# Kernel optimization log

Hardware: AMD Instinct MI355X
Metric: run time of the kernel (lower is better)

The kernel has to match this reference:

```python
import jax, jax.numpy as jnp
import numpy as np

NCA_HIDDEN = 16
N_CODES = 32
EMBED_DIM = 64


def conv2d(x, w, pad, b=None):
    # x: (N, Cin, H, W), w: (Cout, Cin, kh, kw)
    y = jax.lax.conv_general_dilated(
        x, w, window_strides=(1, 1), padding=[(pad, pad), (pad, pad)],
        dimension_numbers=('NCHW', 'OIHW', 'NCHW'))
    if b is not None:
        y = y + b[None, :, None, None]
    return y


def setup_inputs() -> dict:
    key = jax.random.key(0)
    ks = jax.random.split(key, 32)
    rn = lambda k, shp, s=0.05: jax.random.normal(k, shp, dtype=jnp.float32) * s
    H = NCA_HIDDEN
    upd = H * H * 3 * 3  # 2304
    tau = H * H          # 256
    inp = {
        'demo_inputs':  jax.random.normal(ks[0], (8, 1, 64, 64), dtype=jnp.float32),
        'demo_outputs': jax.random.normal(ks[1], (8, 1, 64, 64), dtype=jnp.float32),
        'test_input':   jax.random.normal(ks[2], (16, 1, 256, 256), dtype=jnp.float32),
        # TaskEncoder params
        'enc_w1': rn(ks[3], (16, 2, 3, 3)),  'enc_b1': jnp.zeros((16,), jnp.float32),
        'enc_w2': rn(ks[4], (32, 16, 3, 3)), 'enc_b2': jnp.zeros((32,), jnp.float32),
        'enc_lw': rn(ks[5], (EMBED_DIM, 32)), 'enc_lb': jnp.zeros((EMBED_DIM,), jnp.float32),
        # gen_update hypernet
        'gu_w1': rn(ks[6], (128, EMBED_DIM)), 'gu_b1': jnp.zeros((128,), jnp.float32),
        'gu_w2': rn(ks[7], (upd, 128)),       'gu_b2': jnp.zeros((upd,), jnp.float32),
        # gen_tau hypernet
        'gt_w1': rn(ks[8], (64, EMBED_DIM)),  'gt_b1': jnp.zeros((64,), jnp.float32),
        'gt_w2': rn(ks[9], (tau, 64)),        'gt_b2': jnp.zeros((tau,), jnp.float32),
        # stem
        'stem_w': rn(ks[10], (H, 1, 3, 3)), 'stem_b': jnp.zeros((H,), jnp.float32),
        # VQ codebook, init U(-1/n_codes, 1/n_codes)
        'codebook': jax.random.uniform(ks[11], (N_CODES, H), jnp.float32,
                                       minval=-1.0 / N_CODES, maxval=1.0 / N_CODES),
        # decoder 1x1 conv
        'dec_w': rn(ks[12], (1, H, 1, 1)), 'dec_b': jnp.zeros((1,), jnp.float32),
        'n_steps': 5,
    }
    return inp


def reference(demo_inputs, demo_outputs, test_input,
              enc_w1, enc_b1, enc_w2, enc_b2, enc_lw, enc_lb,
              gu_w1, gu_b1, gu_w2, gu_b2,
              gt_w1, gt_b1, gt_w2, gt_b2,
              stem_w, stem_b, codebook, dec_w, dec_b, n_steps):
    H = NCA_HIDDEN
    # --- Task encoder: mean task embedding over demo pairs ---
    pairs = jnp.concatenate([demo_inputs, demo_outputs], axis=1)  # (N,2,h,w)
    h = jax.nn.relu(conv2d(pairs, enc_w1, 1, enc_b1))
    h = jax.nn.relu(conv2d(h, enc_w2, 1, enc_b2))
    h = h.mean(axis=(2, 3))                   # AdaptiveAvgPool2d(1)+Flatten -> (N,32)
    te = (h @ enc_lw.T + enc_lb).mean(axis=0)  # (embed_dim,)
    # --- Hypernetworks generate NCA weights ---
    W_update = (jax.nn.relu(te @ gu_w1.T + gu_b1) @ gu_w2.T + gu_b2).reshape(H, H, 3, 3)
    W_tau = (jax.nn.relu(te @ gt_w1.T + gt_b1) @ gt_w2.T + gt_b2).reshape(H, H, 1, 1)
    # --- Stem ---
    state = jax.nn.relu(conv2d(test_input, stem_w, 1, stem_b))  # (B,16,Hh,Ww)
    cb_sq = (codebook ** 2).sum(axis=1)  # (n_codes,)
    for _ in range(int(n_steps)):
        delta = jax.nn.relu(conv2d(state, W_update, 1))
        beta = jax.nn.sigmoid(conv2d(state, W_tau, 0))
        state = beta * state + (1.0 - beta) * delta
        # --- VQ step (straight-through) ---
        B, C, Hh, Ww = state.shape
        zf = state.transpose(0, 2, 3, 1).reshape(-1, C)  # (B*Hh*Ww, C)
        dists = (zf ** 2).sum(1, keepdims=True) + cb_sq - 2.0 * (zf @ codebook.T)
        idx = jnp.argmin(dists, axis=1)
        zq = codebook[idx].reshape(B, Hh, Ww, C).transpose(0, 3, 1, 2)
        state = state + jax.lax.stop_gradient(zq - state)
    output = jax.nn.sigmoid(conv2d(state, dec_w, 0, dec_b))
    return output
```

## Files before the change

kernel.cpp:

```cpp
#include <hip/hip_runtime.h>
#include <stdint.h>

#define NPIX 65536
#define NIMG 16

typedef float4 F4;
typedef _Float16 h2v __attribute__((ext_vector_type(2)));
typedef _Float16 h8v __attribute__((ext_vector_type(8)));
typedef float    f4v __attribute__((ext_vector_type(4)));

union H8 { h8v v; h2v p[4]; _Float16 e[8]; };

__device__ __forceinline__ float sigm(float x){ return 1.0f/(1.0f+__expf(-x)); }

#if defined(__has_builtin)
#if __has_builtin(__builtin_amdgcn_rcpf)
#define FRCP(x) __builtin_amdgcn_rcpf(x)
#endif
#endif
#ifndef FRCP
#define FRCP(x) (1.0f/(x))
#endif
__device__ __forceinline__ float sigmf(float x){ return FRCP(1.0f + __expf(-x)); }

__device__ __forceinline__ h2v pkrtz(float a, float b){
  return __builtin_bit_cast(h2v, __builtin_amdgcn_cvt_pkrtz(a,b));
}

#if defined(__has_builtin)
#if __has_builtin(__builtin_amdgcn_fdot2)
#define FDOT2(a,b,c) __builtin_amdgcn_fdot2((a),(b),(c),false)
#endif
#endif
#ifndef FDOT2
#define FDOT2(a,b,c) ((c) + (float)(a)[0]*(float)(b)[0] + (float)(a)[1]*(float)(b)[1])
#endif

__global__ __launch_bounds__(256) void k_prep(
    const float* __restrict__ w2, _Float16* __restrict__ wfragE,
    float* __restrict__ pooled)
{
  int t=threadIdx.x;
  pooled[t]=0.f;
  for(int i=t;i<5120;i+=256){
    int j=i&7, rest=i>>3, lane=rest&63, rest2=rest>>6, ks=rest2%5, b=rest2/5;
    int g=lane>>4, nn=lane&15;
    int k=32*ks+8*g+j;
    float v=0.f;
    if(k<144){
      int tap=2*ks+(g>>1), ci=8*(g&1)+j, co=b*16+nn;
      v=w2[co*144+ci*9+tap];
    }
    wfragE[i]=(_Float16)v;
  }
}

__global__ __launch_bounds__(256) void k_enc(
    const float* __restrict__ din, const float* __restrict__ dou,
    const float* __restrict__ w1, const float* __restrict__ b1,
    const float* __restrict__ b2,
    const _Float16* __restrict__ wfragE,
    float* __restrict__ pooled)
{
  __shared__ float2 in_s[400];
  __shared__ h8v st_h[324*3];
  __shared__ float red[4][32];
  __shared__ h2v stwp_s[144];
  __shared__ h2v stbp_s[8];

  const int tid=threadIdx.x;
  const int bx=blockIdx.x, by=blockIdx.y, n=blockIdx.z;
  const float* i0 = din + n*4096;
  const float* i1 = dou + n*4096;

  for(int i=tid;i<400;i+=256){
    int sy=i/20, sx=i-sy*20;
    int gy=by*16-2+sy, gx=bx*16-2+sx;
    bool ok=((unsigned)gy<64u && (unsigned)gx<64u);
    in_s[i] = ok ? make_float2(i0[gy*64+gx], i1[gy*64+gx]) : make_float2(0.f,0.f);
  }
  if(tid<144){
    int q=tid/18, r=tid-18*q;
    stwp_s[tid]=pkrtz(w1[36*q+r], w1[36*q+18+r]);
  } else if(tid<152){
    int q=tid-144;
    stbp_s[q]=pkrtz(b1[2*q], b1[2*q+1]);
  }

  const int lane=tid&63, w=tid>>6, g=lane>>4, nn=lane&15;
  h8v B0[5], B1[5];
  const h8v* wfE=(const h8v*)wfragE;
  #pragma unroll
  for(int ks=0;ks<5;ks++){ B0[ks]=wfE[ks*64+lane]; B1[ks]=wfE[(5+ks)*64+lane]; }
  float b2a=b2[nn], b2b=b2[nn+16];
  __syncthreads();

  for(int p=tid;p<324;p+=256){
    int syh=p/18, sxh=p-syh*18;
    int gy=by*16-1+syh, gx=bx*16-1+sxh;
    H8 o0,o1;
    if((unsigned)gy<64u && (unsigned)gx<64u){
      h2v a2[8];
      #pragma unroll
      for(int q=0;q<8;q++) a2[q]=stbp_s[q];
      #pragma unroll
      for(int ky=0;ky<3;ky++){
        #pragma unroll
        for(int kx=0;kx<3;kx++){
          int tp=ky*3+kx;
          float2 v=in_s[(syh+ky)*20+(sxh+kx)];
          h2v v0=pkrtz(v.x,v.x), v1=pkrtz(v.y,v.y);
          #pragma unroll
          for(int q=0;q<8;q++){
            a2[q]=stwp_s[(2*q)*9+tp]*v0 + a2[q];
            a2[q]=stwp_s[(2*q+1)*9+tp]*v1 + a2[q];
          }
        }
      }
      o0.p[0]=a2[0]; o0.p[1]=a2[1]; o0.p[2]=a2[2]; o0.p[3]=a2[3];
      o1.p[0]=a2[4]; o1.p[1]=a2[5]; o1.p[2]=a2[6]; o1.p[3]=a2[7];
      #pragma unroll
      for(int c=0;c<8;c++){
        o0.e[c]=o0.e[c]>(_Float16)0?o0.e[c]:(_Float16)0;
        o1.e[c]=o1.e[c]>(_Float16)0?o1.e[c]:(_Float16)0;
      }
    } else {
      o0.v=(h8v){0,0,0,0,0,0,0,0};
      o1.v=(h8v){0,0,0,0,0,0,0,0};
    }
    st_h[p*3]  =o0.v;
    st_h[p*3+1]=o1.v;
  }
  __syncthreads();

  f4v acc0[4], acc1[4];
  #pragma unroll
  for(int m=0;m<4;m++){ acc0[m]=(f4v){0.f,0.f,0.f,0.f}; acc1[m]=(f4v){0.f,0.f,0.f,0.f}; }
  #pragma unroll
  for(int ks=0;ks<5;ks++){
    int t=2*ks+(g>>1); if(t>8) t=8;
    int tyo=(t*11)>>5, txo=t-tyo*3;
    int sel=g&1;
    #pragma unroll
    for(int m=0;m<4;m++){
      int sy=4*w+m+tyo;
      h8v a=st_h[(sy*18+nn+txo)*3+sel];
      acc0[m]=__builtin_amdgcn_mfma_f32_16x16x32_f16(a,B0[ks],acc0[m],0,0,0);
      acc1[m]=__builtin_amdgcn_mfma_f32_16x16x32_f16(a,B1[ks],acc1[m],0,0,0);
    }
  }
  float s0=0.f, s1=0.f;
  #pragma unroll
  for(int m=0;m<4;m++)
    #pragma unroll
    for(int r=0;r<4;r++){
      s0+=fmaxf(acc0[m][r]+b2a,0.f);
      s1+=fmaxf(acc1[m][r]+b2b,0.f);
    }
  s0+=__shfl_down(s0,32,64); s0+=__shfl_down(s0,16,64);
  s1+=__shfl_down(s1,32,64); s1+=__shfl_down(s1,16,64);
  if(lane<16){ red[w][nn]=s0; red[w][nn+16]=s1; }
  __syncthreads();
  if(tid<32){
    float s=red[0][tid]+red[1][tid]+red[2][tid]+red[3][tid];
    atomicAdd(&pooled[n*32+tid], s);
  }
}

__global__ __launch_bounds__(256) void k_hyper(
    const float* __restrict__ pooled,
    const float* __restrict__ lw, const float* __restrict__ lb,
    const float* __restrict__ guw1, const float* __restrict__ gub1,
    const float* __restrict__ gtw1, const float* __restrict__ gtb1,
    const float* __restrict__ gtw2, const float* __restrict__ gtb2,
    const float* __restrict__ guw2, const float* __restrict__ gub2,
    const float* __restrict__ cb, const float* __restrict__ decw, const float* __restrict__ decb,
    _Float16* __restrict__ wfrag_g,
    _Float16* __restrict__ Mh_g,
    _Float16* __restrict__ bcb_g, _Float16* __restrict__ omb_g,
    _Float16* __restrict__ cbh_g,
    float* __restrict__ chs_g, float* __restrict__ dvals_g)
{
  __shared__ float hm[32], te_s[64], hx_s[128];
  __shared__ float wz_s[256];
  __shared__ float cb_s[512];
  const int t=threadIdx.x, blk=blockIdx.x;
  if(t<32){
    float s=0.f;
    for(int n=0;n<8;n++) s += pooled[n*32+t];
    hm[t] = s * (1.0f/32768.0f);
  }
  for(int i=t;i<512;i+=256) cb_s[i]=cb[i];
  if(blk==9){
    for(int i=t;i<5120;i+=256){
      int j=i&7, rest=i>>3, lane=rest&63, rest2=rest>>6, ks=rest2%5, b=rest2/5;
      int k=32*ks+8*(lane>>4)+j;
      bool pad = (b==0) ? (k>=144) : ((k>>4)!=4);
      if(pad) wfrag_g[i]=(_Float16)0.f;
    }
    for(int i=t;i<264;i+=256){ int k=i>>3, q=i&7; Mh_g[k*152+144+q]=(_Float16)0.f; }
    for(int i=t;i<144;i+=256) Mh_g[32*152+i]=(_Float16)0.f;
  }
  __syncthreads();
  if(t<64){
    float s=lb[t];
    for(int c=0;c<32;c++) s = fmaf(lw[t*32+c], hm[c], s);
    te_s[t]=s;
  }
  __syncthreads();
  if(blk<9){
    if(t<128){
      float s=gub1[t];
      for(int j=0;j<64;j++) s = fmaf(guw1[t*64+j], te_s[j], s);
      hx_s[t]=fmaxf(s,0.f);
    }
    __syncthreads();
    const int ci=t>>4, co=t&15, tp=blk;
    const int o=co*144+ci*9+tp;
    float s=gub2[o];
    const F4* gp=(const F4*)(guw2+(size_t)o*128);
    #pragma unroll
    for(int i=0;i<32;i++){
      F4 g=gp[i];
      s=fmaf(g.x,hx_s[4*i],s); s=fmaf(g.y,hx_s[4*i+1],s);
      s=fmaf(g.z,hx_s[4*i+2],s); s=fmaf(g.w,hx_s[4*i+3],s);
    }
    wz_s[ci*16+co]=s;
    {
      int k=tp*16+ci;
      int ks=k>>5, rem=k&31, g2=rem>>3, j=rem&7, lane=(g2<<4)|co;
      wfrag_g[(ks*64+lane)*8+j]=(_Float16)s;
    }
    __syncthreads();
    for(int o2=t;o2<512;o2+=256){
      int k=o2>>4, c=o2&15;
      float m=0.f;
      for(int c2=0;c2<16;c2++) m=fmaf(wz_s[c2*16+c], cb_s[k*16+c2], m);
      Mh_g[k*152+tp*16+c]=(_Float16)m;
    }
  } else {
    if(t<64){
      float s=gtb1[t];
      for(int j=0;j<64;j++) s = fmaf(gtw1[t*64+j], te_s[j], s);
      hx_s[t]=fmaxf(s,0.f);
    }
    __syncthreads();
    {
      float s=gtb2[t];
      for(int i=0;i<64;i++) s = fmaf(gtw2[t*64+i], hx_s[i], s);
      int co=t>>4, ci=t&15;
      wz_s[ci*16+co]=s;
    }
    __syncthreads();
    {
      int ci=t>>4, co=t&15;
      int g=ci>>3, j=ci&7, lane=(g<<4)|co;
      wfrag_g[(448+lane)*8+j]=(_Float16)wz_s[ci*16+co];
    }
    for(int o=t;o<512;o+=256){
      int k=o>>4, c=o&15;
      float T=0.f;
      for(int ci=0;ci<16;ci++) T = fmaf(wz_s[ci*16+c], cb_s[k*16+ci], T);
      float beta=sigm(T);
      bcb_g[o]=(_Float16)(beta*cb_s[o]);
      omb_g[o]=(_Float16)(1.f-beta);
      cbh_g[o]=(_Float16)cb_s[o];
    }
    if(t<32){
      float sq=0.f, d=0.f;
      for(int c=0;c<16;c++){ float v=cb_s[t*16+c]; sq=fmaf(v,v,sq); d=fmaf(decw[c],v,d); }
      chs_g[t]=0.5f*sq;
      dvals_g[t]=sigm(d+decb[0]);
    }
  }
}

#define ST_STRIDE 3
struct S1P1 { h8v st[324*ST_STRIDE]; float in[400]; };
union S1U { S1P1 p; unsigned int dt[256*20]; };

__global__ __launch_bounds__(256) void k_step1(
    const float* __restrict__ tin,
    const float* __restrict__ stw, const float* __restrict__ stb,
    const _Float16* __restrict__ wfrag,
    const _Float16* __restrict__ cbh, const float* __restrict__ chs,
    uint8_t* __restrict__ idx_out)
{
  __shared__ S1U u;
  __shared__ h8v cb8_s[64];
  __shared__ float chs_s[32];
  __shared__ h2v stwp_s[72];
  __shared__ h2v stbp_s[8];

  const int tid=threadIdx.x;
  const int bx=blockIdx.x, by=blockIdx.y, n=blockIdx.z;
  const float* in = tin + (size_t)n*NPIX;

  for(int i=tid;i<400;i+=256){
    int sy=i/20, sx=i-sy*20;
    int gy=by*16-2+sy, gx=bx*16-2+sx;
    u.p.in[i] = ((unsigned)gy<256u && (unsigned)gx<256u) ? in[gy*256+gx] : 0.0f;
  }
  if(tid<72){
    int q=tid/9, tp=tid-q*9;
    stwp_s[q*9+tp]=pkrtz(stw[(2*q)*9+tp], stw[(2*q+1)*9+tp]);
  } else if(tid<80){
    int q=tid-72;
    stbp_s[q]=pkrtz(stb[2*q], stb[2*q+1]);
  } else if(tid>=160 && tid<192) chs_s[tid-160]=chs[tid-160];
  if(tid<64) ((uint4*)cb8_s)[tid] = ((const uint4*)cbh)[tid];

  const int lane = tid & 63, w = tid >> 6;
  const int g = lane >> 4, nn = lane & 15;
  h8v Bd[5], Bt2;
  const h8v* wf = (const h8v*)wfrag;
  #pragma unroll
  for(int ks=0;ks<5;ks++) Bd[ks]=wf[ks*64+lane];
  Bt2 = wf[7*64+lane];

  __syncthreads();

  for(int p=tid;p<324;p+=256){
    int syh=p/18, sxh=p-syh*18;
    int gy=by*16-1+syh, gx=bx*16-1+sxh;
    H8 b0,b1;
    if((unsigned)gy<256u && (unsigned)gx<256u){
      h2v a2[8];
      #pragma unroll
      for(int q=0;q<8;q++) a2[q]=stbp_s[q];
      #pragma unroll
      for(int ky=0;ky<3;ky++){
        #pragma unroll
        for(int kx=0;kx<3;kx++){
          int tp=ky*3+kx;
          float v=u.p.in[(syh+ky)*20+(sxh+kx)];
          h2v vv=pkrtz(v,v);
          #pragma unroll
          for(int q=0;q<8;q++) a2[q] = stwp_s[q*9+tp]*vv + a2[q];
        }
      }
      b0.p[0]=a2[0]; b0.p[1]=a2[1]; b0.p[2]=a2[2]; b0.p[3]=a2[3];
      b1.p[0]=a2[4]; b1.p[1]=a2[5]; b1.p[2]=a2[6]; b1.p[3]=a2[7];
      #pragma unroll
      for(int c=0;c<8;c++){
        b0.e[c]=b0.e[c]>(_Float16)0?b0.e[c]:(_Float16)0;
        b1.e[c]=b1.e[c]>(_Float16)0?b1.e[c]:(_Float16)0;
      }
    } else {
      b0.v=(h8v){0,0,0,0,0,0,0,0};
      b1.v=(h8v){0,0,0,0,0,0,0,0};
    }
    u.p.st[p*ST_STRIDE]  =b0.v;
    u.p.st[p*ST_STRIDE+1]=b1.v;
  }
  __syncthreads();

  f4v accd[4], acct[4];
  #pragma unroll
  for(int m=0;m<4;m++){ accd[m]=(f4v){0.f,0.f,0.f,0.f}; acct[m]=(f4v){0.f,0.f,0.f,0.f}; }
  #pragma unroll
  for(int ks=0;ks<5;ks++){
    int t = 2*ks + (g>>1); if(t>8) t=8;
    int tyo=(t*11)>>5, txo=t-tyo*3;
    int sel = g&1;
    #pragma unroll
    for(int m=0;m<4;m++){
      int sy = 4*w+m+tyo;
      h8v a = u.p.st[(sy*18 + nn + txo)*ST_STRIDE + sel];
      accd[m]=__builtin_amdgcn_mfma_f32_16x16x32_f16(a,Bd[ks],accd[m],0,0,0);
      if(ks==2) acct[m]=__builtin_amdgcn_mfma_f32_16x16x32_f16(a,Bt2,acct[m],0,0,0);
    }
  }
  const int py=tid>>4, pxx=tid&15;
  const int cpx=((py+1)*18+pxx+1)*ST_STRIDE;
  h8v z0=u.p.st[cpx], z1=u.p.st[cpx+1];
  __syncthreads();

  #pragma unroll
  for(int m=0;m<4;m++){
    #pragma unroll
    for(int r=0;r<4;r++){
      int px=(4*w+m)*16 + g*4 + r;
      h2v pk = pkrtz(accd[m][r], acct[m][r]);
      u.dt[px*20+nn] = __builtin_bit_cast(unsigned int, pk);
    }
  }
  __syncthreads();

  const uint4* dr=(const uint4*)(u.dt+tid*20);
  uint4 q0=dr[0],q1=dr[1],q2=dr[2],q3=dr[3];
  unsigned int qq[16]={q0.x,q0.y,q0.z,q0.w,q1.x,q1.y,q1.z,q1.w,
                       q2.x,q2.y,q2.z,q2.w,q3.x,q3.y,q3.z,q3.w};
  float zn[16];
  #pragma unroll
  for(int c=0;c<16;c++){
    h2v dt2=__builtin_bit_cast(h2v, qq[c]);
    float d=(float)dt2[0]; d = d>0.f?d:0.f;
    float beta=sigmf((float)dt2[1]);
    float zv = (c<8)? (float)z0[c] : (float)z1[c-8];
    zn[c]=fmaf(beta, zv-d, d);
  }
  H8 u0,u1;
  #pragma unroll
  for(int j=0;j<4;j++){
    u0.p[j]=pkrtz(zn[2*j],zn[2*j+1]);
    u1.p[j]=pkrtz(zn[8+2*j],zn[9+2*j]);
  }
  int best=0; float bv=-3.4e38f;
  #pragma unroll
  for(int k=0;k<32;k++){
    H8 c0,c1; c0.v=cb8_s[k*2]; c1.v=cb8_s[k*2+1];
    float dot=0.f;
    #pragma unroll
    for(int j=0;j<4;j++) dot=FDOT2(u0.p[j],c0.p[j],dot);
    #pragma unroll
    for(int j=0;j<4;j++) dot=FDOT2(u1.p[j],c1.p[j],dot);
    float val=dot-chs_s[k];
    if(val>bv){bv=val;best=k;}
  }
  idx_out[(size_t)n*NPIX + (by*16+py)*256 + (bx*16+pxx)]=(uint8_t)best;
}

__global__ __launch_bounds__(256) void k_stepN(
    const uint8_t* __restrict__ idx_in,
    const uint4* __restrict__ Mh,
    const _Float16* __restrict__ bcbh, const _Float16* __restrict__ ombh,
    const _Float16* __restrict__ cbh,  const float* __restrict__ chs,
    const float* __restrict__ dvals,
    uint8_t* __restrict__ idx_out, float* __restrict__ out, int last)
{
  __shared__ int id_s[324];
  __shared__ uint4 M_s[627];
  __shared__ h8v bcb_s[64], omb_s[64], cb8_s[64];
  __shared__ float chs_s[32], dv_s[32];
  const int tid=threadIdx.x;
  const int bx=blockIdx.x, by=blockIdx.y, n=blockIdx.z;
  const uint8_t* ip = idx_in + (size_t)n*NPIX;

  for(int i=tid;i<324;i+=256){
    int sy=i/18, sx=i-sy*18;
    int gy=by*16-1+sy, gx=bx*16-1+sx;
    id_s[i] = ((unsigned)gy<256u && (unsigned)gx<256u) ? (int)ip[gy*256+gx] : 32;
  }
  for(int i=tid;i<627;i+=256) M_s[i]=Mh[i];
  if(tid<64)        ((uint4*)bcb_s)[tid]     = ((const uint4*)bcbh)[tid];
  else if(tid<128)  ((uint4*)omb_s)[tid-64]  = ((const uint4*)ombh)[tid-64];
  else if(tid<192)  ((uint4*)cb8_s)[tid-128] = ((const uint4*)cbh)[tid-128];
  else if(tid<224)  chs_s[tid-192]=chs[tid-192];
  else              dv_s[tid-224]=dvals[tid-224];
  __syncthreads();

  const int py=tid>>4, pxx=tid&15;
  int ida[9];
  #pragma unroll
  for(int dy=0;dy<3;dy++)
    #pragma unroll
    for(int dx=0;dx<3;dx++)
      ida[dy*3+dx]=id_s[(py+dy)*18+pxx+dx];

  const h8v* Mv=(const h8v*)M_s;
  h8v a0={0,0,0,0,0,0,0,0}, a1={0,0,0,0,0,0,0,0};
  #pragma unroll
  for(int t=0;t<9;t++){
    const h8v* mp=&Mv[ida[t]*19+t*2];
    a0+=mp[0]; a1+=mp[1];
  }
  int kc=ida[4];
  h8v r0,r1;
  #pragma unroll
  for(int q=0;q<8;q++){
    r0[q]=a0[q]>(_Float16)0?a0[q]:(_Float16)0;
    r1[q]=a1[q]>(_Float16)0?a1[q]:(_Float16)0;
  }
  H8 u0,u1;
  u0.v = bcb_s[kc*2]   + omb_s[kc*2]  *r0;
  u1.v = bcb_s[kc*2+1] + omb_s[kc*2+1]*r1;
  int best=0; float bv=-3.4e38f;
  #pragma unroll
  for(int k=0;k<32;k++){
    H8 c0,c1; c0.v=cb8_s[k*2]; c1.v=cb8_s[k*2+1];
    float dot=0.f;
    #pragma unroll
    for(int j=0;j<4;j++) dot=FDOT2(u0.p[j],c0.p[j],dot);
    #pragma unroll
    for(int j=0;j<4;j++) dot=FDOT2(u1.p[j],c1.p[j],dot);
    float val=dot-chs_s[k];
    if(val>bv){bv=val;best=k;}
  }
  size_t gidx=(size_t)n*NPIX + (size_t)(by*16+py)*256 + bx*16+pxx;
  if(last) out[gidx]=dv_s[best];
  else     idx_out[gidx]=(uint8_t)best;
}

extern "C" void kernel_launch(void* const* d_in, const int* in_sizes, int n_in,
                              void* d_out, int out_size, void* d_ws, size_t ws_size,
                              hipStream_t stream)
{
  const float* demo_in  = (const float*)d_in[0];
  const float* demo_out = (const float*)d_in[1];
  const float* test_in  = (const float*)d_in[2];
  const float* enc_w1 = (const float*)d_in[3];
  const float* enc_b1 = (const float*)d_in[4];
  const float* enc_w2 = (const float*)d_in[5];
  const float* enc_b2 = (const float*)d_in[6];
  const float* enc_lw = (const float*)d_in[7];
  const float* enc_lb = (const float*)d_in[8];
  const float* gu_w1 = (const float*)d_in[9];
  const float* gu_b1 = (const float*)d_in[10];
  const float* gu_w2 = (const float*)d_in[11];
  const float* gu_b2 = (const float*)d_in[12];
  const float* gt_w1 = (const float*)d_in[13];
  const float* gt_b1 = (const float*)d_in[14];
  const float* gt_w2 = (const float*)d_in[15];
  const float* gt_b2 = (const float*)d_in[16];
  const float* stem_w = (const float*)d_in[17];
  const float* stem_b = (const float*)d_in[18];
  const float* codebook = (const float*)d_in[19];
  const float* dec_w = (const float*)d_in[20];
  const float* dec_b = (const float*)d_in[21];

  float* ws = (float*)d_ws;
  float* pooled = ws;
  float* chs    = pooled + 256;
  float* dvals  = chs + 32;
  float* hid_g  = dvals + 32;
  _Float16* hbase = (_Float16*)(ws + 448);
  _Float16* wfrag  = hbase;
  _Float16* wfragE = hbase + 5120;
  _Float16* Mh     = hbase + 10240;
  _Float16* bcbh   = hbase + 15264;
  _Float16* ombh   = hbase + 15776;
  _Float16* cbh    = hbase + 16288;
  uint8_t* idxA = (uint8_t*)(hbase + 16800);
  uint8_t* idxB = idxA + (size_t)NIMG*NPIX;
  (void)hid_g;

  k_prep<<<1,256,0,stream>>>(enc_w2, wfragE, pooled);
  k_enc<<<dim3(4,4,8),256,0,stream>>>(demo_in, demo_out, enc_w1, enc_b1, enc_b2, wfragE, pooled);
  k_hyper<<<10,256,0,stream>>>(pooled, enc_lw, enc_lb,
                               gu_w1,gu_b1, gt_w1,gt_b1, gt_w2,gt_b2,
                               gu_w2,gu_b2, codebook, dec_w, dec_b,
                               wfrag, Mh, bcbh, ombh, cbh, chs, dvals);
  dim3 tgrid(16,16,NIMG);
  k_step1<<<tgrid,256,0,stream>>>(test_in, stem_w, stem_b, wfrag, cbh, chs, idxA);
  float* outp = (float*)d_out;
  k_stepN<<<tgrid,256,0,stream>>>(idxA,(const uint4*)Mh,bcbh,ombh,cbh,chs,dvals, idxB,outp,0);
  k_stepN<<<tgrid,256,0,stream>>>(idxB,(const uint4*)Mh,bcbh,ombh,cbh,chs,dvals, idxA,outp,0);
  k_stepN<<<tgrid,256,0,stream>>>(idxA,(const uint4*)Mh,bcbh,ombh,cbh,chs,dvals, idxB,outp,0);
  k_stepN<<<tgrid,256,0,stream>>>(idxB,(const uint4*)Mh,bcbh,ombh,cbh,chs,dvals, idxA,outp,1);
}
```

Baseline: 244.3 us.

## Compute VQ codebook distances in stepN with MFMA instead of scalar dot2

The per-pixel nearest-codeword search in k_stepN moves from 32 scalar fdot2 loops per thread onto MFMA 16x16x32 f16 instructions. k_hyper prebuilds codebook A-fragments, and each thread stages its updated state vector in LDS so each wave can process 16 pixels per MFMA pair. An argmin across lanes via shuffles picks the best code with lowest-index tie-breaking. This trades scalar ALU work for extra LDS traffic, shuffles and a 4-round loop per wave.

```diff
diff --git a/kernel.cpp b/kernel.cpp
--- a/kernel.cpp
+++ b/kernel.cpp
@@ -179,6 +179,7 @@
     _Float16* __restrict__ Mh_g,
     _Float16* __restrict__ bcb_g, _Float16* __restrict__ omb_g,
     _Float16* __restrict__ cbh_g,
+    _Float16* __restrict__ vqA_g,
     float* __restrict__ chs_g, float* __restrict__ dvals_g)
 {
   __shared__ float hm[32], te_s[64], hx_s[128];
@@ -256,6 +257,12 @@
       int ci=t>>4, co=t&15;
       int g=ci>>3, j=ci&7, lane=(g<<4)|co;
       wfrag_g[(448+lane)*8+j]=(_Float16)wz_s[ci*16+co];
+    }
+    for(int i=t;i<1024;i+=256){
+      int j=i&7, lane=(i>>3)&63, c=i>>9;
+      int g=lane>>4, m=lane&15, k=g*8+j;
+      float v=(k<16)? cb_s[(c*16+m)*16+k] : 0.f;
+      vqA_g[i]=(_Float16)v;
     }
     for(int o=t;o<512;o+=256){
       int k=o>>4, c=o&15;
@@ -425,14 +432,15 @@
     const uint8_t* __restrict__ idx_in,
     const uint4* __restrict__ Mh,
     const _Float16* __restrict__ bcbh, const _Float16* __restrict__ ombh,
-    const _Float16* __restrict__ cbh,  const float* __restrict__ chs,
+    const _Float16* __restrict__ vqA,  const float* __restrict__ chs,
     const float* __restrict__ dvals,
     uint8_t* __restrict__ idx_out, float* __restrict__ out, int last)
 {
   __shared__ int id_s[324];
   __shared__ uint4 M_s[627];
-  __shared__ h8v bcb_s[64], omb_s[64], cb8_s[64];
+  __shared__ h8v bcb_s[64], omb_s[64];
   __shared__ float chs_s[32], dv_s[32];
+  __shared__ h8v zn_s[256*3];
   const int tid=threadIdx.x;
   const int bx=blockIdx.x, by=blockIdx.y, n=blockIdx.z;
   const uint8_t* ip = idx_in + (size_t)n*NPIX;
@@ -445,10 +453,15 @@
   for(int i=tid;i<627;i+=256) M_s[i]=Mh[i];
   if(tid<64)        ((uint4*)bcb_s)[tid]     = ((const uint4*)bcbh)[tid];
   else if(tid<128)  ((uint4*)omb_s)[tid-64]  = ((const uint4*)ombh)[tid-64];
-  else if(tid<192)  ((uint4*)cb8_s)[tid-128] = ((const uint4*)cbh)[tid-128];
-  else if(tid<224)  chs_s[tid-192]=chs[tid-192];
-  else              dv_s[tid-224]=dvals[tid-224];
-  __syncthreads();
+  else if(tid<160)  chs_s[tid-128]=chs[tid-128];
+  else if(tid<192)  dv_s[tid-160]=dvals[tid-160];
+
+  const int lane=tid&63, w=tid>>6, g=lane>>4, nn=lane&15;
+  h8v A0=((const h8v*)vqA)[lane], A1=((const h8v*)vqA)[64+lane];
+  __syncthreads();
+  f4v C0,C1;
+  #pragma unroll
+  for(int r=0;r<4;r++){ C0[r]=-chs_s[4*g+r]; C1[r]=-chs_s[16+4*g+r]; }
 
   const int py=tid>>4, pxx=tid&15;
   int ida[9];
@@ -472,21 +485,43 @@
     r0[q]=a0[q]>(_Float16)0?a0[q]:(_Float16)0;
     r1[q]=a1[q]>(_Float16)0?a1[q]:(_Float16)0;
   }
-  H8 u0,u1;
-  u0.v = bcb_s[kc*2]   + omb_s[kc*2]  *r0;
-  u1.v = bcb_s[kc*2+1] + omb_s[kc*2+1]*r1;
-  int best=0; float bv=-3.4e38f;
-  #pragma unroll
-  for(int k=0;k<32;k++){
-    H8 c0,c1; c0.v=cb8_s[k*2]; c1.v=cb8_s[k*2+1];
-    float dot=0.f;
-    #pragma unroll
-    for(int j=0;j<4;j++) dot=FDOT2(u0.p[j],c0.p[j],dot);
-    #pragma unroll
-    for(int j=0;j<4;j++) dot=FDOT2(u1.p[j],c1.p[j],dot);
-    float val=dot-chs_s[k];
-    if(val>bv){bv=val;best=k;}
-  }
+  h8v zn0 = bcb_s[kc*2]   + omb_s[kc*2]  *r0;
+  h8v zn1 = bcb_s[kc*2+1] + omb_s[kc*2+1]*r1;
+  zn_s[tid*3]  =zn0;
+  zn_s[tid*3+1]=zn1;
+  __builtin_amdgcn_wave_barrier();
+
+  int best=0; float bdummy;
+  (void)bdummy;
+  #pragma unroll
+  for(int b=0;b<4;b++){
+    h8v Bf=(h8v){0,0,0,0,0,0,0,0};
+    if(g<2) Bf=zn_s[(w*64+b*16+nn)*3+g];
+    f4v D0=__builtin_amdgcn_mfma_f32_16x16x32_f16(A0,Bf,C0,0,0,0);
+    f4v D1=__builtin_amdgcn_mfma_f32_16x16x32_f16(A1,Bf,C1,0,0,0);
+    float lv=-3.4e38f; int li=99;
+    #pragma unroll
+    for(int r=0;r<4;r++){
+      float v=D0[r]; int ii=4*g+r;
+      bool tk=(v>lv)||((v==lv)&&(ii<li));
+      lv=tk?v:lv; li=tk?ii:li;
+    }
+    #pragma unroll
+    for(int r=0;r<4;r++){
+      float v=D1[r]; int ii=16+4*g+r;
+      bool tk=(v>lv)||((v==lv)&&(ii<li));
+      lv=tk?v:lv; li=tk?ii:li;
+    }
+    #pragma unroll
+    for(int mm=16;mm<=32;mm<<=1){
+      float vo=__shfl_xor(lv,mm,64);
+      int io=__shfl_xor(li,mm,64);
+      bool tk=(vo>lv)||((vo==lv)&&(io<li));
+      lv=tk?vo:lv; li=tk?io:li;
+    }
+    if(g==b) best=li;
+  }
+
   size_t gidx=(size_t)n*NPIX + (size_t)(by*16+py)*256 + bx*16+pxx;
   if(last) out[gidx]=dv_s[best];
   else     idx_out[gidx]=(uint8_t)best;
@@ -531,7 +566,8 @@
   _Float16* bcbh   = hbase + 15264;
   _Float16* ombh   = hbase + 15776;
   _Float16* cbh    = hbase + 16288;
-  uint8_t* idxA = (uint8_t*)(hbase + 16800);
+  _Float16* vqA    = hbase + 16800;
+  uint8_t* idxA = (uint8_t*)(hbase + 17824);
   uint8_t* idxB = idxA + (size_t)NIMG*NPIX;
   (void)hid_g;
 
@@ -540,12 +576,12 @@
   k_hyper<<<10,256,0,stream>>>(pooled, enc_lw, enc_lb,
                                gu_w1,gu_b1, gt_w1,gt_b1, gt_w2,gt_b2,
                                gu_w2,gu_b2, codebook, dec_w, dec_b,
-                               wfrag, Mh, bcbh, ombh, cbh, chs, dvals);
+                               wfrag, Mh, bcbh, ombh, cbh, vqA, chs, dvals);
   dim3 tgrid(16,16,NIMG);
   k_step1<<<tgrid,256,0,stream>>>(test_in, stem_w, stem_b, wfrag, cbh, chs, idxA);
   float* outp = (float*)d_out;
-  k_stepN<<<tgrid,256,0,stream>>>(idxA,(const uint4*)Mh,bcbh,ombh,cbh,chs,dvals, idxB,outp,0);
-  k_stepN<<<tgrid,256,0,stream>>>(idxB,(const uint4*)Mh,bcbh,ombh,cbh,chs,dvals, idxA,outp,0);
-  k_stepN<<<tgrid,256,0,stream>>>(idxA,(const uint4*)Mh,bcbh,ombh,cbh,chs,dvals, idxB,outp,0);
-  k_stepN<<<tgrid,256,0,stream>>>(idxB,(const uint4*)Mh,bcbh,ombh,cbh,chs,dvals, idxA,outp,1);
-}
+  k_stepN<<<tgrid,256,0,stream>>>(idxA,(const uint4*)Mh,bcbh,ombh,vqA,chs,dvals, idxB,outp,0);
+  k_stepN<<<tgrid,256,0,stream>>>(idxB,(const uint4*)Mh,bcbh,ombh,vqA,chs,dvals, idxA,outp,0);
+  k_stepN<<<tgrid,256,0,stream>>>(idxA,(const uint4*)Mh,bcbh,ombh,vqA,chs,dvals, idxB,outp,0);
+  k_stepN<<<tgrid,256,0,stream>>>(idxB,(const uint4*)Mh,bcbh,ombh,vqA,chs,dvals, idxA,outp,1);
+}
```

Measured after the change: 239.6 us. About the same (-1.9%).

## Fuse four NCA step launches into one cooperative persistent kernel with grid sync

Applied to the files above, without the earlier changes.

Replaces the four separate k_stepN launches with a single cooperative kernel of 1024 blocks. Each block processes four 16x16 tiles per step and uses grid.sync between steps, ping-ponging between the index buffers. Shared constants (M table, codebook, biases) are loaded once per block instead of once per tile per step, and three kernel launch gaps are removed. In exchange it depends on all 1024 blocks being co-resident for the cooperative launch, and it pays the cost of grid-wide barriers.

```diff
diff --git a/kernel.cpp b/kernel.cpp
--- a/kernel.cpp
+++ b/kernel.cpp
@@ -1,5 +1,8 @@
 #include <hip/hip_runtime.h>
+#include <hip/hip_cooperative_groups.h>
 #include <stdint.h>
+
+namespace cg = cooperative_groups;
 
 #define NPIX 65536
 #define NIMG 16
@@ -421,75 +424,89 @@
   idx_out[(size_t)n*NPIX + (by*16+py)*256 + (bx*16+pxx)]=(uint8_t)best;
 }
 
-__global__ __launch_bounds__(256) void k_stepN(
-    const uint8_t* __restrict__ idx_in,
+__global__ __launch_bounds__(256) void k_steps(
+    uint8_t* __restrict__ idxA, uint8_t* __restrict__ idxB,
     const uint4* __restrict__ Mh,
     const _Float16* __restrict__ bcbh, const _Float16* __restrict__ ombh,
     const _Float16* __restrict__ cbh,  const float* __restrict__ chs,
     const float* __restrict__ dvals,
-    uint8_t* __restrict__ idx_out, float* __restrict__ out, int last)
+    float* __restrict__ out)
 {
   __shared__ int id_s[324];
   __shared__ uint4 M_s[627];
   __shared__ h8v bcb_s[64], omb_s[64], cb8_s[64];
   __shared__ float chs_s[32], dv_s[32];
   const int tid=threadIdx.x;
-  const int bx=blockIdx.x, by=blockIdx.y, n=blockIdx.z;
-  const uint8_t* ip = idx_in + (size_t)n*NPIX;
-
-  for(int i=tid;i<324;i+=256){
-    int sy=i/18, sx=i-sy*18;
-    int gy=by*16-1+sy, gx=bx*16-1+sx;
-    id_s[i] = ((unsigned)gy<256u && (unsigned)gx<256u) ? (int)ip[gy*256+gx] : 32;
-  }
+
   for(int i=tid;i<627;i+=256) M_s[i]=Mh[i];
   if(tid<64)        ((uint4*)bcb_s)[tid]     = ((const uint4*)bcbh)[tid];
   else if(tid<128)  ((uint4*)omb_s)[tid-64]  = ((const uint4*)ombh)[tid-64];
   else if(tid<192)  ((uint4*)cb8_s)[tid-128] = ((const uint4*)cbh)[tid-128];
   else if(tid<224)  chs_s[tid-192]=chs[tid-192];
   else              dv_s[tid-224]=dvals[tid-224];
-  __syncthreads();
-
+
+  const h8v* Mv=(const h8v*)M_s;
   const int py=tid>>4, pxx=tid&15;
-  int ida[9];
-  #pragma unroll
-  for(int dy=0;dy<3;dy++)
-    #pragma unroll
-    for(int dx=0;dx<3;dx++)
-      ida[dy*3+dx]=id_s[(py+dy)*18+pxx+dx];
-
-  const h8v* Mv=(const h8v*)M_s;
-  h8v a0={0,0,0,0,0,0,0,0}, a1={0,0,0,0,0,0,0,0};
-  #pragma unroll
-  for(int t=0;t<9;t++){
-    const h8v* mp=&Mv[ida[t]*19+t*2];
-    a0+=mp[0]; a1+=mp[1];
-  }
-  int kc=ida[4];
-  h8v r0,r1;
-  #pragma unroll
-  for(int q=0;q<8;q++){
-    r0[q]=a0[q]>(_Float16)0?a0[q]:(_Float16)0;
-    r1[q]=a1[q]>(_Float16)0?a1[q]:(_Float16)0;
-  }
-  H8 u0,u1;
-  u0.v = bcb_s[kc*2]   + omb_s[kc*2]  *r0;
-  u1.v = bcb_s[kc*2+1] + omb_s[kc*2+1]*r1;
-  int best=0; float bv=-3.4e38f;
-  #pragma unroll
-  for(int k=0;k<32;k++){
-    H8 c0,c1; c0.v=cb8_s[k*2]; c1.v=cb8_s[k*2+1];
-    float dot=0.f;
-    #pragma unroll
-    for(int j=0;j<4;j++) dot=FDOT2(u0.p[j],c0.p[j],dot);
-    #pragma unroll
-    for(int j=0;j<4;j++) dot=FDOT2(u1.p[j],c1.p[j],dot);
-    float val=dot-chs_s[k];
-    if(val>bv){bv=val;best=k;}
-  }
-  size_t gidx=(size_t)n*NPIX + (size_t)(by*16+py)*256 + bx*16+pxx;
-  if(last) out[gidx]=dv_s[best];
-  else     idx_out[gidx]=(uint8_t)best;
+  cg::grid_group grid = cg::this_grid();
+
+  for(int s=0;s<4;s++){
+    const uint8_t* src = (s&1)? idxB : idxA;
+    uint8_t*       dst = (s&1)? idxA : idxB;
+    const bool lastS = (s==3);
+    #pragma unroll 1
+    for(int it=0; it<4; it++){
+      int tile = blockIdx.x*4+it;
+      int n = tile>>8, rem=tile&255, by=rem>>4, bx=rem&15;
+      const uint8_t* ip = src + (size_t)n*NPIX;
+      __syncthreads();
+      for(int i=tid;i<324;i+=256){
+        int sy=i/18, sx=i-sy*18;
+        int gy=by*16-1+sy, gx=bx*16-1+sx;
+        id_s[i] = ((unsigned)gy<256u && (unsigned)gx<256u) ? (int)ip[gy*256+gx] : 32;
+      }
+      __syncthreads();
+
+      int ida[9];
+      #pragma unroll
+      for(int dy=0;dy<3;dy++)
+        #pragma unroll
+        for(int dx=0;dx<3;dx++)
+          ida[dy*3+dx]=id_s[(py+dy)*18+pxx+dx];
+
+      h8v a0={0,0,0,0,0,0,0,0}, a1={0,0,0,0,0,0,0,0};
+      #pragma unroll
+      for(int t=0;t<9;t++){
+        const h8v* mp=&Mv[ida[t]*19+t*2];
+        a0+=mp[0]; a1+=mp[1];
+      }
+      int kc=ida[4];
+      h8v r0,r1;
+      #pragma unroll
+      for(int q=0;q<8;q++){
+        r0[q]=a0[q]>(_Float16)0?a0[q]:(_Float16)0;
+        r1[q]=a1[q]>(_Float16)0?a1[q]:(_Float16)0;
+      }
+      H8 u0,u1;
+      u0.v = bcb_s[kc*2]   + omb_s[kc*2]  *r0;
+      u1.v = bcb_s[kc*2+1] + omb_s[kc*2+1]*r1;
+      int best=0; float bv=-3.4e38f;
+      #pragma unroll
+      for(int k=0;k<32;k++){
+        H8 c0,c1; c0.v=cb8_s[k*2]; c1.v=cb8_s[k*2+1];
+        float dot=0.f;
+        #pragma unroll
+        for(int j=0;j<4;j++) dot=FDOT2(u0.p[j],c0.p[j],dot);
+        #pragma unroll
+        for(int j=0;j<4;j++) dot=FDOT2(u1.p[j],c1.p[j],dot);
+        float val=dot-chs_s[k];
+        if(val>bv){bv=val;best=k;}
+      }
+      size_t gidx=(size_t)n*NPIX + (size_t)(by*16+py)*256 + bx*16+pxx;
+      if(lastS) out[gidx]=dv_s[best];
+      else      dst[gidx]=(uint8_t)best;
+    }
+    if(s<3) grid.sync();
+  }
 }
 
 extern "C" void kernel_launch(void* const* d_in, const int* in_sizes, int n_in,
@@ -544,8 +561,10 @@
   dim3 tgrid(16,16,NIMG);
   k_step1<<<tgrid,256,0,stream>>>(test_in, stem_w, stem_b, wfrag, cbh, chs, idxA);
   float* outp = (float*)d_out;
-  k_stepN<<<tgrid,256,0,stream>>>(idxA,(const uint4*)Mh,bcbh,ombh,cbh,chs,dvals, idxB,outp,0);
-  k_stepN<<<tgrid,256,0,stream>>>(idxB,(const uint4*)Mh,bcbh,ombh,cbh,chs,dvals, idxA,outp,0);
-  k_stepN<<<tgrid,256,0,stream>>>(idxA,(const uint4*)Mh,bcbh,ombh,cbh,chs,dvals, idxB,outp,0);
-  k_stepN<<<tgrid,256,0,stream>>>(idxB,(const uint4*)Mh,bcbh,ombh,cbh,chs,dvals, idxA,outp,1);
-}
+  const uint4* Mh4 = (const uint4*)Mh;
+  void* kargs[] = { (void*)&idxA, (void*)&idxB, (void*)&Mh4,
+                    (void*)&bcbh, (void*)&ombh, (void*)&cbh,
+                    (void*)&chs, (void*)&dvals, (void*)&outp };
+  (void)hipLaunchCooperativeKernel((void*)k_steps, dim3(1024), dim3(256),
+                                   kargs, 0, stream);
+}
```

Result: slower. 602.8 us (+146.7%).
